# Kernel optimization log

Hardware: AMD Instinct MI355X
Metric: run time of the kernel (lower is better)

Reference implementation:

```python
import jax, jax.numpy as jnp
import numpy as np

SPARSE_COMPRESSION_RATIO = 0.5  # config.sparse_compression_ratio


def setup_inputs() -> dict:
    key = jax.random.key(0)
    kv_cache = jax.random.normal(key, (2, 32, 4096, 128), dtype=jnp.float32)
    return {"kv_cache": kv_cache}


def reference(kv_cache):
    # elements_to_keep = int(numel * (1 - ratio))
    total = kv_cache.size
    k = int(total * (1.0 - SPARSE_COMPRESSION_RATIO))
    flat = kv_cache.reshape(-1)
    # torch.topk(|x|, k, largest=True) -> indices of k largest magnitudes
    _, top_idx = jax.lax.top_k(jnp.abs(flat), k)
    # scatter mask, then elementwise multiply (zeros out non-top-k entries)
    mask = jnp.zeros((total,), dtype=jnp.bool_).at[top_idx].set(True)
    return kv_cache * mask.reshape(kv_cache.shape)
```

## Files before the change

### kernel.cpp

```cpp
#include <hip/hip_runtime.h>
#include <stdint.h>


#define NTHR 256
#define MASK31 0x7fffffffu

typedef unsigned int v4u __attribute__((ext_vector_type(4)));

#define SH_OFF    0
#define SH_BINS   8192
#define CH_OFF    8192
#define CH_BINS   4096
#define SCL_OFF   12288
#define L3_OFF    12304
#define L3_CAP    4096
#define PAIRS_OFF (L3_OFF + 2 * L3_CAP)
#define PAIRS_CAP (1u << 20)
#define ZERO_WORDS (SCL_OFF + 16)

#define STG_CAP   2048

__global__ void zero_ws_kernel(uint32_t* __restrict__ ws) {
    int i = blockIdx.x * blockDim.x + threadIdx.x;
    if (i < ZERO_WORDS) ws[i] = 0;
}

__global__ void sample_hist_kernel(const uint4* __restrict__ xv, long long n4,
                                   uint32_t* __restrict__ ws) {
    __shared__ uint32_t lh[SH_BINS];
    for (int i = threadIdx.x; i < SH_BINS; i += NTHR) lh[i] = 0;
    __syncthreads();
    long long chunkStride = n4 >> 7;
    long long base = (long long)blockIdx.x * chunkStride + threadIdx.x;
    for (int j = 0; j < 8; ++j) {
        long long idx = base + (long long)j * NTHR;
        if (idx < n4) {
            uint4 v = xv[idx];
            atomicAdd(&lh[(v.x & MASK31) >> 18], 1u);
            atomicAdd(&lh[(v.y & MASK31) >> 18], 1u);
            atomicAdd(&lh[(v.z & MASK31) >> 18], 1u);
            atomicAdd(&lh[(v.w & MASK31) >> 18], 1u);
        }
    }
    __syncthreads();
    for (int i = threadIdx.x; i < SH_BINS; i += NTHR)
        if (lh[i]) atomicAdd(&ws[SH_OFF + i], lh[i]);
}

__global__ void sel_bracket_kernel(uint32_t* __restrict__ ws,
                                   uint32_t ksmM, uint32_t kspM) {
    __shared__ uint32_t lh[SH_BINS];
    __shared__ uint32_t csum[NTHR];
    __shared__ uint32_t cpre[NTHR];
    __shared__ int sBHi, sB1;
    for (int i = threadIdx.x; i < SH_BINS; i += NTHR) lh[i] = ws[SH_OFF + i];
    if (threadIdx.x == 0) { sBHi = -1; sB1 = -1; }
    __syncthreads();
    uint32_t s = 0;
    for (int i = 0; i < 32; ++i) s += lh[threadIdx.x * 32 + i];
    csum[threadIdx.x] = s;
    __syncthreads();
    if (threadIdx.x == 0) {
        uint32_t run = 0;
        for (int c = NTHR - 1; c >= 0; --c) { cpre[c] = run; run += csum[c]; }
    }
    __syncthreads();
    {
        int c = threadIdx.x;
        int hitHi = -1, hitB1 = -1;
        uint32_t excl = cpre[c];
        for (int bb = c * 32 + 31; bb >= c * 32; --bb) {
            uint32_t cnt = lh[bb];
            uint32_t incl = excl + cnt;
            if (hitHi < 0 && incl >= ksmM) hitHi = bb;
            if (hitB1 < 0 && excl >= kspM) hitB1 = bb;
            excl = incl;
        }
        if (hitHi >= 0) atomicMax(&sBHi, hitHi);
        if (hitB1 >= 0) atomicMax(&sB1, hitB1);
    }
    __syncthreads();
    if (threadIdx.x == 0) {
        int bHi = sBHi < 0 ? 0 : sBHi;
        int bLo = sB1 + 1;
        if (bLo > bHi) bLo = bHi;
        if (bLo < 0) bLo = 0;
        int sbins = bHi - bLo + 1;
        int clog = 0; while ((1 << clog) < sbins) ++clog;
        int spanBits = 18 + clog;
        int shift1 = spanBits - 12;
        if (shift1 < 0) shift1 = 0;
        ws[SCL_OFF + 0] = ((uint32_t)bLo) << 18;
        ws[SCL_OFF + 1] = ((uint32_t)(bHi + 1)) << 18;
        ws[SCL_OFF + 2] = (uint32_t)shift1;
    }
}

__global__ __launch_bounds__(NTHR, 4)
void fused_main_kernel(const uint32_t* __restrict__ x,
                       uint32_t* __restrict__ out, long long n,
                       uint32_t* __restrict__ ws) {
    __shared__ uint2 stage[STG_CAP];
    __shared__ uint32_t cnt, sBase, redHi[NTHR / 64];
    const uint32_t uLo = ws[SCL_OFF + 0];
    const uint32_t uHi = ws[SCL_OFF + 1];
    const uint32_t span = uHi - uLo;
    if (threadIdx.x == 0) cnt = 0u;
    __syncthreads();

    const v4u* __restrict__ xv = (const v4u*)x;
    v4u* __restrict__ ov = (v4u*)out;
    uint2* __restrict__ gpairs = (uint2*)(ws + PAIRS_OFF);
    long long n4 = n >> 2;
    const long long stride = (long long)gridDim.x * NTHR;
    const long long i0 = (long long)blockIdx.x * NTHR + threadIdx.x;

    uint32_t myHi = 0;
    uint32_t hitMask = 0;
    uint32_t it = 0;
    long long i = i0;

#define CLASS(v, o, hb) { \
    uint32_t c0 = v.x & MASK31, c1 = v.y & MASK31, c2 = v.z & MASK31, c3 = v.w & MASK31; \
    myHi += (uint32_t)(c0 >= uHi) + (uint32_t)(c1 >= uHi) \
          + (uint32_t)(c2 >= uHi) + (uint32_t)(c3 >= uHi); \
    o.x = (c0 >= uHi) ? v.x : 0u; o.y = (c1 >= uHi) ? v.y : 0u; \
    o.z = (c2 >= uHi) ? v.z : 0u; o.w = (c3 >= uHi) ? v.w : 0u; \
    hb = (uint32_t)((c0 - uLo) < span) | (uint32_t)((c1 - uLo) < span) \
       | (uint32_t)((c2 - uLo) < span) | (uint32_t)((c3 - uLo) < span); }

    for (; i + 3 * stride < n4; i += 4 * stride, it += 4) {
        v4u v0 = xv[i];
        v4u v1 = xv[i + stride];
        v4u v2 = xv[i + 2 * stride];
        v4u v3 = xv[i + 3 * stride];
        v4u o0, o1, o2, o3;
        uint32_t h0, h1, h2, h3;
        CLASS(v0, o0, h0) CLASS(v1, o1, h1) CLASS(v2, o2, h2) CLASS(v3, o3, h3)
        hitMask |= h0 << (it & 31);
        hitMask |= h1 << ((it + 1) & 31);
        hitMask |= h2 << ((it + 2) & 31);
        hitMask |= h3 << ((it + 3) & 31);
        __builtin_nontemporal_store(o0, &ov[i]);
        __builtin_nontemporal_store(o1, &ov[i + stride]);
        __builtin_nontemporal_store(o2, &ov[i + 2 * stride]);
        __builtin_nontemporal_store(o3, &ov[i + 3 * stride]);
    }
    for (; i < n4; i += stride, ++it) {
        v4u v = xv[i];
        v4u o;
        uint32_t hb;
        CLASS(v, o, hb)
        hitMask |= hb << (it & 31);
        __builtin_nontemporal_store(o, &ov[i]);
    }
#undef CLASS

#define PUSHP(val, eidx) { \
    uint32_t p_ = atomicAdd(&cnt, 1u); \
    uint2 pr_ = make_uint2((val), (eidx)); \
    if (p_ < STG_CAP) stage[p_] = pr_; \
    else { uint32_t g_ = atomicAdd(&ws[SCL_OFF + 4], 1u); \
           if (g_ < PAIRS_CAP) gpairs[g_] = pr_; } }

    if (blockIdx.x == 0) {
        for (long long idx = (n4 << 2) + threadIdx.x; idx < n; idx += NTHR) {
            uint32_t v = x[idx];
            uint32_t u = v & MASK31;
            myHi += (uint32_t)(u >= uHi);
            if (u - uLo < span) PUSHP(v, (uint32_t)idx)
            out[idx] = (u >= uHi) ? v : 0u;
        }
    }

    while (hitMask) {
        uint32_t b = __ffs(hitMask) - 1u;
        hitMask &= hitMask - 1u;
        for (long long ii = i0 + (long long)b * stride; ii < n4; ii += (stride << 5)) {
            v4u v = xv[ii];
            uint32_t e0 = (uint32_t)(ii << 2);
            uint32_t u;
            u = v.x & MASK31; if (u - uLo < span) PUSHP(v.x, e0 + 0u)
            u = v.y & MASK31; if (u - uLo < span) PUSHP(v.y, e0 + 1u)
            u = v.z & MASK31; if (u - uLo < span) PUSHP(v.z, e0 + 2u)
            u = v.w & MASK31; if (u - uLo < span) PUSHP(v.w, e0 + 3u)
        }
    }
#undef PUSHP

    for (int o = 32; o > 0; o >>= 1) myHi += __shfl_down(myHi, o);
    if ((threadIdx.x & 63) == 0) redHi[threadIdx.x >> 6] = myHi;
    __syncthreads();
    if (threadIdx.x == 0) {
        uint32_t tot = 0;
        for (int w = 0; w < NTHR / 64; ++w) tot += redHi[w];
        if (tot) atomicAdd(&ws[SCL_OFF + 3], tot);
        uint32_t c = cnt < STG_CAP ? cnt : STG_CAP;
        cnt = c;
        sBase = atomicAdd(&ws[SCL_OFF + 4], c);
    }
    __syncthreads();
    uint32_t c = cnt, bw = sBase;
    for (uint32_t q = threadIdx.x; q < c; q += NTHR)
        if (bw + q < PAIRS_CAP) gpairs[bw + q] = stage[q];
}

__global__ void cand_hist_kernel(uint32_t* __restrict__ ws) {
    __shared__ uint32_t lh[CH_BINS];
    uint32_t G = ws[SCL_OFF + 4]; if (G > PAIRS_CAP) G = PAIRS_CAP;
    uint32_t uLo = ws[SCL_OFF + 0], shift1 = ws[SCL_OFF + 2];
    for (int i = threadIdx.x; i < CH_BINS; i += NTHR) lh[i] = 0;
    __syncthreads();
    const uint2* pairs = (const uint2*)(ws + PAIRS_OFF);
    uint32_t stride = gridDim.x * NTHR;
    for (uint32_t i = blockIdx.x * NTHR + threadIdx.x; i < G; i += stride) {
        uint32_t u = pairs[i].x & MASK31;
        atomicAdd(&lh[((u - uLo) >> shift1) & (CH_BINS - 1)], 1u);
    }
    __syncthreads();
    for (int i = threadIdx.x; i < CH_BINS; i += NTHR)
        if (lh[i]) atomicAdd(&ws[CH_OFF + i], lh[i]);
}

__global__ void sel_gather_kernel(uint32_t* __restrict__ ws, uint32_t k) {
    __shared__ uint32_t lh[CH_BINS];
    __shared__ uint32_t csum[NTHR];
    __shared__ uint32_t cpre[NTHR];
    __shared__ uint32_t sBase2, sRem2, sKp;
    for (int i = threadIdx.x; i < CH_BINS; i += NTHR) lh[i] = ws[CH_OFF + i];
    __syncthreads();
    uint32_t s = 0;
    for (int i = 0; i < 16; ++i) s += lh[threadIdx.x * 16 + i];
    csum[threadIdx.x] = s;
    __syncthreads();
    if (threadIdx.x == 0) {
        uint32_t run = 0;
        for (int c = NTHR - 1; c >= 0; --c) { cpre[c] = run; run += csum[c]; }
        uint32_t cntHi = ws[SCL_OFF + 3];
        uint32_t total = cpre[0] + csum[0];
        uint32_t kp = (k > cntHi) ? (k - cntHi) : 1u;
        if (kp > total) kp = total;
        if (kp < 1u) kp = 1u;
        sKp = kp;
    }
    __syncthreads();
    uint32_t kp = sKp;
    if (cpre[threadIdx.x] < kp && kp <= cpre[threadIdx.x] + csum[threadIdx.x]) {
        uint32_t excl = cpre[threadIdx.x];
        for (int bb = threadIdx.x * 16 + 15; bb >= threadIdx.x * 16; --bb) {
            uint32_t cnt = lh[bb];
            if (excl + cnt >= kp) {
                sBase2 = ws[SCL_OFF + 0] + (((uint32_t)bb) << ws[SCL_OFF + 2]);
                sRem2 = kp - excl;
                break;
            }
            excl += cnt;
        }
    }
    __syncthreads();
    if (threadIdx.x == 0) { ws[SCL_OFF + 5] = sBase2; ws[SCL_OFF + 6] = sRem2; }
    uint32_t base2 = sBase2;
    uint32_t width = 1u << ws[SCL_OFF + 2];
    uint32_t G = ws[SCL_OFF + 4]; if (G > PAIRS_CAP) G = PAIRS_CAP;
    const uint2* pairs = (const uint2*)(ws + PAIRS_OFF);
    uint2* l3 = (uint2*)(ws + L3_OFF);
    uint32_t stride = gridDim.x * NTHR;
    for (uint32_t i = blockIdx.x * NTHR + threadIdx.x; i < G; i += stride) {
        uint2 pr = pairs[i];
        uint32_t u = pr.x & MASK31;
        if (u - base2 < width) {
            uint32_t p = atomicAdd(&ws[SCL_OFF + 7], 1u);
            if (p < L3_CAP) l3[p] = pr;
        }
    }
}

__global__ void final_fixup_kernel(uint32_t* __restrict__ ws,
                                   uint32_t* __restrict__ out) {
    __shared__ uint2 l3s[L3_CAP];
    uint32_t c3 = ws[SCL_OFF + 7]; if (c3 > L3_CAP) c3 = L3_CAP;
    uint32_t base2 = ws[SCL_OFF + 5], rem2 = ws[SCL_OFF + 6];
    uint32_t width = 1u << ws[SCL_OFF + 2];
    uint32_t tHi2 = base2 + width;
    const uint2* l3 = (const uint2*)(ws + L3_OFF);
    for (uint32_t q = threadIdx.x; q < c3; q += NTHR) l3s[q] = l3[q];
    __syncthreads();
    uint32_t G = ws[SCL_OFF + 4]; if (G > PAIRS_CAP) G = PAIRS_CAP;
    const uint2* pairs = (const uint2*)(ws + PAIRS_OFF);
    uint32_t stride = gridDim.x * NTHR;
    for (uint32_t i = blockIdx.x * NTHR + threadIdx.x; i < G; i += stride) {
        uint2 pr = pairs[i];
        uint32_t u = pr.x & MASK31;
        if (u >= tHi2) {
            out[pr.y] = pr.x;
        } else if (u - base2 < width) {
            uint32_t rank = 0;
            for (uint32_t p = 0; p < c3; ++p) {
                uint2 q2 = l3s[p];
                uint32_t up = q2.x & MASK31;
                rank += (up > u || (up == u && q2.y < pr.y)) ? 1u : 0u;
            }
            if (rank < rem2) out[pr.y] = pr.x;
        }
    }
}

extern "C" void kernel_launch(void* const* d_in, const int* in_sizes, int n_in,
                              void* d_out, int out_size, void* d_ws, size_t ws_size,
                              hipStream_t stream) {
    const uint32_t* x = (const uint32_t*)d_in[0];
    uint32_t* out = (uint32_t*)d_out;
    uint32_t* ws = (uint32_t*)d_ws;
    long long n = (long long)in_sizes[0];

    const double ratio = 0.5;
    long long k = (long long)((double)n * (1.0 - ratio));
    if (k < 1) k = 1;
    if (k > n) k = n;

    long long n4 = n >> 2;
    long long S = ((n4 >> 7) >= 2048) ? (128LL * NTHR * 8 * 4)
                                      : (n4 << 2);
    long long ks = (long long)((double)k * ((double)S / (double)n));
    const long long M = 4500;
    uint32_t ksmM = (uint32_t)((ks - M) < 1 ? 1 : (ks - M));
    uint32_t kspM = (uint32_t)((ks + M) > S ? S : (ks + M));

    long long nBlk = (n4 + (long long)NTHR * 16 - 1) / ((long long)NTHR * 16);
    if (nBlk < 1) nBlk = 1;
    if (nBlk > 8192) nBlk = 8192;
    int grid = (int)nBlk;

    zero_ws_kernel<<<(ZERO_WORDS + NTHR - 1) / NTHR, NTHR, 0, stream>>>(ws);
    sample_hist_kernel<<<128, NTHR, 0, stream>>>((const uint4*)x, n4, ws);
    sel_bracket_kernel<<<1, NTHR, 0, stream>>>(ws, ksmM, kspM);
    fused_main_kernel<<<grid, NTHR, 0, stream>>>(x, out, n, ws);
    cand_hist_kernel<<<256, NTHR, 0, stream>>>(ws);
    sel_gather_kernel<<<256, NTHR, 0, stream>>>(ws, (uint32_t)k);
    final_fixup_kernel<<<256, NTHR, 0, stream>>>(ws, out);
}
```

Baseline: 143.2 us.

## Replace global atomic candidate compaction with per-block segments and larger sample

```diff
diff --git a/kernel.cpp b/kernel.cpp
--- a/kernel.cpp
+++ b/kernel.cpp
@@ -12,30 +12,36 @@
 #define CH_OFF    8192
 #define CH_BINS   4096
 #define SCL_OFF   12288
-#define L3_OFF    12304
-#define L3_CAP    4096
-#define PAIRS_OFF (L3_OFF + 2 * L3_CAP)
-#define PAIRS_CAP (1u << 20)
-#define ZERO_WORDS (SCL_OFF + 16)
-
-#define STG_CAP   2048
+#define ZERO_WORDS (SCL_OFF + 32)
+#define HIC_OFF   12320
+#define PCN_OFF   14368
+#define L3C_OFF   16416
+#define L3S_OFF   16672
+#define L3SEG_CAP 64
+#define OVFP_OFF  49440
+#define OVFP_CAP  16384
+#define OVL3_OFF  90000
+#define OVL3_CAP  2048
+#define PAIRS_OFF 131072
+#define SEG_CAP   2048
+#define NBLK_MAIN 2048
 
 __global__ void zero_ws_kernel(uint32_t* __restrict__ ws) {
     int i = blockIdx.x * blockDim.x + threadIdx.x;
     if (i < ZERO_WORDS) ws[i] = 0;
 }
 
-__global__ void sample_hist_kernel(const uint4* __restrict__ xv, long long n4,
+__global__ void sample_hist_kernel(const v4u* __restrict__ xv, long long n4,
                                    uint32_t* __restrict__ ws) {
     __shared__ uint32_t lh[SH_BINS];
     for (int i = threadIdx.x; i < SH_BINS; i += NTHR) lh[i] = 0;
     __syncthreads();
-    long long chunkStride = n4 >> 7;
-    long long base = (long long)blockIdx.x * chunkStride + threadIdx.x;
-    for (int j = 0; j < 8; ++j) {
-        long long idx = base + (long long)j * NTHR;
-        if (idx < n4) {
-            uint4 v = xv[idx];
+    long long S4 = n4 >> 3;
+    long long T = (long long)gridDim.x * NTHR;
+    for (long long s = (long long)blockIdx.x * NTHR + threadIdx.x; s < S4; s += T) {
+        long long idx4 = ((s >> 9) << 12) | (s & 511);
+        if (idx4 < n4) {
+            v4u v = xv[idx4];
             atomicAdd(&lh[(v.x & MASK31) >> 18], 1u);
             atomicAdd(&lh[(v.y & MASK31) >> 18], 1u);
             atomicAdd(&lh[(v.z & MASK31) >> 18], 1u);
@@ -96,12 +102,11 @@
     }
 }
 
-__global__ __launch_bounds__(NTHR, 4)
-void fused_main_kernel(const uint32_t* __restrict__ x,
-                       uint32_t* __restrict__ out, long long n,
-                       uint32_t* __restrict__ ws) {
-    __shared__ uint2 stage[STG_CAP];
-    __shared__ uint32_t cnt, sBase, redHi[NTHR / 64];
+__global__ void fused_main_kernel(const uint32_t* __restrict__ x,
+                                  uint32_t* __restrict__ out, long long n,
+                                  uint32_t* __restrict__ ws) {
+    __shared__ uint2 stage[SEG_CAP];
+    __shared__ uint32_t cnt, redHi[NTHR / 64];
     const uint32_t uLo = ws[SCL_OFF + 0];
     const uint32_t uHi = ws[SCL_OFF + 1];
     const uint32_t span = uHi - uLo;
@@ -110,7 +115,6 @@
 
     const v4u* __restrict__ xv = (const v4u*)x;
     v4u* __restrict__ ov = (v4u*)out;
-    uint2* __restrict__ gpairs = (uint2*)(ws + PAIRS_OFF);
     long long n4 = n >> 2;
     const long long stride = (long long)gridDim.x * NTHR;
     const long long i0 = (long long)blockIdx.x * NTHR + threadIdx.x;
@@ -156,12 +160,13 @@
     }
 #undef CLASS
 
+    uint2* __restrict__ ovfp = (uint2*)(ws + OVFP_OFF);
 #define PUSHP(val, eidx) { \
     uint32_t p_ = atomicAdd(&cnt, 1u); \
     uint2 pr_ = make_uint2((val), (eidx)); \
-    if (p_ < STG_CAP) stage[p_] = pr_; \
-    else { uint32_t g_ = atomicAdd(&ws[SCL_OFF + 4], 1u); \
-           if (g_ < PAIRS_CAP) gpairs[g_] = pr_; } }
+    if (p_ < SEG_CAP) stage[p_] = pr_; \
+    else { uint32_t g_ = atomicAdd(&ws[SCL_OFF + 5], 1u); \
+           if (g_ < OVFP_CAP) ovfp[g_] = pr_; } }
 
     if (blockIdx.x == 0) {
         for (long long idx = (n4 << 2) + threadIdx.x; idx < n; idx += NTHR) {
@@ -194,28 +199,39 @@
     if (threadIdx.x == 0) {
         uint32_t tot = 0;
         for (int w = 0; w < NTHR / 64; ++w) tot += redHi[w];
-        if (tot) atomicAdd(&ws[SCL_OFF + 3], tot);
-        uint32_t c = cnt < STG_CAP ? cnt : STG_CAP;
+        ws[HIC_OFF + blockIdx.x] = tot;
+        uint32_t c = cnt < SEG_CAP ? cnt : SEG_CAP;
         cnt = c;
-        sBase = atomicAdd(&ws[SCL_OFF + 4], c);
-    }
-    __syncthreads();
-    uint32_t c = cnt, bw = sBase;
-    for (uint32_t q = threadIdx.x; q < c; q += NTHR)
-        if (bw + q < PAIRS_CAP) gpairs[bw + q] = stage[q];
+        ws[PCN_OFF + blockIdx.x] = c;
+    }
+    __syncthreads();
+    uint2* __restrict__ seg = (uint2*)(ws + PAIRS_OFF) + (size_t)blockIdx.x * SEG_CAP;
+    uint32_t c = cnt;
+    for (uint32_t q = threadIdx.x; q < c; q += NTHR) seg[q] = stage[q];
 }
 
 __global__ void cand_hist_kernel(uint32_t* __restrict__ ws) {
     __shared__ uint32_t lh[CH_BINS];
-    uint32_t G = ws[SCL_OFF + 4]; if (G > PAIRS_CAP) G = PAIRS_CAP;
     uint32_t uLo = ws[SCL_OFF + 0], shift1 = ws[SCL_OFF + 2];
     for (int i = threadIdx.x; i < CH_BINS; i += NTHR) lh[i] = 0;
     __syncthreads();
     const uint2* pairs = (const uint2*)(ws + PAIRS_OFF);
-    uint32_t stride = gridDim.x * NTHR;
-    for (uint32_t i = blockIdx.x * NTHR + threadIdx.x; i < G; i += stride) {
-        uint32_t u = pairs[i].x & MASK31;
-        atomicAdd(&lh[((u - uLo) >> shift1) & (CH_BINS - 1)], 1u);
+    for (int g = 0; g < NBLK_MAIN / 256; ++g) {
+        uint32_t sidx = blockIdx.x + (uint32_t)g * 256u;
+        uint32_t c = ws[PCN_OFF + sidx];
+        const uint2* seg = pairs + (size_t)sidx * SEG_CAP;
+        for (uint32_t i = threadIdx.x; i < c; i += NTHR) {
+            uint32_t u = seg[i].x & MASK31;
+            atomicAdd(&lh[((u - uLo) >> shift1) & (CH_BINS - 1)], 1u);
+        }
+    }
+    if (blockIdx.x == 0) {
+        uint32_t c = ws[SCL_OFF + 5]; if (c > OVFP_CAP) c = OVFP_CAP;
+        const uint2* ovfp = (const uint2*)(ws + OVFP_OFF);
+        for (uint32_t i = threadIdx.x; i < c; i += NTHR) {
+            uint32_t u = ovfp[i].x & MASK31;
+            atomicAdd(&lh[((u - uLo) >> shift1) & (CH_BINS - 1)], 1u);
+        }
     }
     __syncthreads();
     for (int i = threadIdx.x; i < CH_BINS; i += NTHR)
@@ -226,8 +242,17 @@
     __shared__ uint32_t lh[CH_BINS];
     __shared__ uint32_t csum[NTHR];
     __shared__ uint32_t cpre[NTHR];
-    __shared__ uint32_t sBase2, sRem2, sKp;
+    __shared__ uint32_t sBase2, sRem2, sKp, lcnt;
+    uint32_t part = 0;
+    for (int i = threadIdx.x; i < NBLK_MAIN; i += NTHR) part += ws[HIC_OFF + i];
+    for (int o = 32; o > 0; o >>= 1) part += __shfl_down(part, o);
     for (int i = threadIdx.x; i < CH_BINS; i += NTHR) lh[i] = ws[CH_OFF + i];
+    if (threadIdx.x == 0) lcnt = 0;
+    csum[threadIdx.x] = 0;
+    __syncthreads();
+    if ((threadIdx.x & 63) == 0) csum[threadIdx.x >> 6] = part;
+    __syncthreads();
+    uint32_t cntHi = csum[0] + csum[1] + csum[2] + csum[3];
     __syncthreads();
     uint32_t s = 0;
     for (int i = 0; i < 16; ++i) s += lh[threadIdx.x * 16 + i];
@@ -236,7 +261,6 @@
     if (threadIdx.x == 0) {
         uint32_t run = 0;
         for (int c = NTHR - 1; c >= 0; --c) { cpre[c] = run; run += csum[c]; }
-        uint32_t cntHi = ws[SCL_OFF + 3];
         uint32_t total = cpre[0] + csum[0];
         uint32_t kp = (k > cntHi) ? (k - cntHi) : 1u;
         if (kp > total) kp = total;
@@ -258,49 +282,110 @@
         }
     }
     __syncthreads();
-    if (threadIdx.x == 0) { ws[SCL_OFF + 5] = sBase2; ws[SCL_OFF + 6] = sRem2; }
+    if (threadIdx.x == 0) { ws[SCL_OFF + 3] = sBase2; ws[SCL_OFF + 4] = sRem2; }
     uint32_t base2 = sBase2;
     uint32_t width = 1u << ws[SCL_OFF + 2];
-    uint32_t G = ws[SCL_OFF + 4]; if (G > PAIRS_CAP) G = PAIRS_CAP;
     const uint2* pairs = (const uint2*)(ws + PAIRS_OFF);
-    uint2* l3 = (uint2*)(ws + L3_OFF);
-    uint32_t stride = gridDim.x * NTHR;
-    for (uint32_t i = blockIdx.x * NTHR + threadIdx.x; i < G; i += stride) {
-        uint2 pr = pairs[i];
-        uint32_t u = pr.x & MASK31;
-        if (u - base2 < width) {
-            uint32_t p = atomicAdd(&ws[SCL_OFF + 7], 1u);
-            if (p < L3_CAP) l3[p] = pr;
-        }
-    }
-}
-
+    uint2* myl3 = (uint2*)(ws + L3S_OFF) + (size_t)blockIdx.x * L3SEG_CAP;
+    uint2* ovl3 = (uint2*)(ws + OVL3_OFF);
+    __shared__ uint2 lstage[L3SEG_CAP];
+    for (int g = 0; g < NBLK_MAIN / 256; ++g) {
+        uint32_t sidx = blockIdx.x + (uint32_t)g * 256u;
+        uint32_t c = ws[PCN_OFF + sidx];
+        const uint2* seg = pairs + (size_t)sidx * SEG_CAP;
+        for (uint32_t i = threadIdx.x; i < c; i += NTHR) {
+            uint2 pr = seg[i];
+            if ((pr.x & MASK31) - base2 < width) {
+                uint32_t p = atomicAdd(&lcnt, 1u);
+                if (p < L3SEG_CAP) lstage[p] = pr;
+                else { uint32_t g2 = atomicAdd(&ws[SCL_OFF + 6], 1u);
+                       if (g2 < OVL3_CAP) ovl3[g2] = pr; }
+            }
+        }
+    }
+    if (blockIdx.x == 0) {
+        uint32_t c = ws[SCL_OFF + 5]; if (c > OVFP_CAP) c = OVFP_CAP;
+        const uint2* ovfp = (const uint2*)(ws + OVFP_OFF);
+        for (uint32_t i = threadIdx.x; i < c; i += NTHR) {
+            uint2 pr = ovfp[i];
+            if ((pr.x & MASK31) - base2 < width) {
+                uint32_t p = atomicAdd(&lcnt, 1u);
+                if (p < L3SEG_CAP) lstage[p] = pr;
+                else { uint32_t g2 = atomicAdd(&ws[SCL_OFF + 6], 1u);
+                       if (g2 < OVL3_CAP) ovl3[g2] = pr; }
+            }
+        }
+    }
+    __syncthreads();
+    uint32_t c = lcnt < L3SEG_CAP ? lcnt : L3SEG_CAP;
+    if (threadIdx.x == 0) ws[L3C_OFF + blockIdx.x] = c;
+    for (uint32_t q = threadIdx.x; q < c; q += NTHR) myl3[q] = lstage[q];
+}
+
+#define L3TOT_CAP 4096
 __global__ void final_fixup_kernel(uint32_t* __restrict__ ws,
                                    uint32_t* __restrict__ out) {
-    __shared__ uint2 l3s[L3_CAP];
-    uint32_t c3 = ws[SCL_OFF + 7]; if (c3 > L3_CAP) c3 = L3_CAP;
-    uint32_t base2 = ws[SCL_OFF + 5], rem2 = ws[SCL_OFF + 6];
+    __shared__ uint2 l3s[L3TOT_CAP];
+    __shared__ uint32_t tc;
+    uint32_t base2 = ws[SCL_OFF + 3], rem2 = ws[SCL_OFF + 4];
     uint32_t width = 1u << ws[SCL_OFF + 2];
     uint32_t tHi2 = base2 + width;
-    const uint2* l3 = (const uint2*)(ws + L3_OFF);
-    for (uint32_t q = threadIdx.x; q < c3; q += NTHR) l3s[q] = l3[q];
-    __syncthreads();
-    uint32_t G = ws[SCL_OFF + 4]; if (G > PAIRS_CAP) G = PAIRS_CAP;
+    if (threadIdx.x == 0) tc = 0;
+    __syncthreads();
+    const uint2* l3seg = (const uint2*)(ws + L3S_OFF);
+    for (int s2 = threadIdx.x; s2 < 256; s2 += NTHR) {
+        uint32_t c = ws[L3C_OFF + s2];
+        uint32_t p = atomicAdd(&tc, c);
+        for (uint32_t q = 0; q < c; ++q)
+            if (p + q < L3TOT_CAP) l3s[p + q] = l3seg[(size_t)s2 * L3SEG_CAP + q];
+    }
+    if (threadIdx.x == 0) {
+        uint32_t c = ws[SCL_OFF + 6]; if (c > OVL3_CAP) c = OVL3_CAP;
+        uint32_t p = atomicAdd(&tc, c);
+        const uint2* ovl3 = (const uint2*)(ws + OVL3_OFF);
+        for (uint32_t q = 0; q < c; ++q)
+            if (p + q < L3TOT_CAP) l3s[p + q] = ovl3[q];
+    }
+    __syncthreads();
+    uint32_t c3 = tc < L3TOT_CAP ? tc : L3TOT_CAP;
     const uint2* pairs = (const uint2*)(ws + PAIRS_OFF);
-    uint32_t stride = gridDim.x * NTHR;
-    for (uint32_t i = blockIdx.x * NTHR + threadIdx.x; i < G; i += stride) {
-        uint2 pr = pairs[i];
-        uint32_t u = pr.x & MASK31;
-        if (u >= tHi2) {
-            out[pr.y] = pr.x;
-        } else if (u - base2 < width) {
-            uint32_t rank = 0;
-            for (uint32_t p = 0; p < c3; ++p) {
-                uint2 q2 = l3s[p];
-                uint32_t up = q2.x & MASK31;
-                rank += (up > u || (up == u && q2.y < pr.y)) ? 1u : 0u;
+    for (int g = 0; g < NBLK_MAIN / 256; ++g) {
+        uint32_t sidx = blockIdx.x + (uint32_t)g * 256u;
+        uint32_t c = ws[PCN_OFF + sidx];
+        const uint2* seg = pairs + (size_t)sidx * SEG_CAP;
+        for (uint32_t i = threadIdx.x; i < c; i += NTHR) {
+            uint2 pr = seg[i];
+            uint32_t u = pr.x & MASK31;
+            if (u >= tHi2) {
+                out[pr.y] = pr.x;
+            } else if (u - base2 < width) {
+                uint32_t rank = 0;
+                for (uint32_t p = 0; p < c3; ++p) {
+                    uint2 q2 = l3s[p];
+                    uint32_t up = q2.x & MASK31;
+                    rank += (up > u || (up == u && q2.y < pr.y)) ? 1u : 0u;
+                }
+                if (rank < rem2) out[pr.y] = pr.x;
             }
-            if (rank < rem2) out[pr.y] = pr.x;
+        }
+    }
+    if (blockIdx.x == 0) {
+        uint32_t c = ws[SCL_OFF + 5]; if (c > OVFP_CAP) c = OVFP_CAP;
+        const uint2* ovfp = (const uint2*)(ws + OVFP_OFF);
+        for (uint32_t i = threadIdx.x; i < c; i += NTHR) {
+            uint2 pr = ovfp[i];
+            uint32_t u = pr.x & MASK31;
+            if (u >= tHi2) {
+                out[pr.y] = pr.x;
+            } else if (u - base2 < width) {
+                uint32_t rank = 0;
+                for (uint32_t p = 0; p < c3; ++p) {
+                    uint2 q2 = l3s[p];
+                    uint32_t up = q2.x & MASK31;
+                    rank += (up > u || (up == u && q2.y < pr.y)) ? 1u : 0u;
+                }
+                if (rank < rem2) out[pr.y] = pr.x;
+            }
         }
     }
 }
@@ -319,22 +404,17 @@
     if (k > n) k = n;
 
     long long n4 = n >> 2;
-    long long S = ((n4 >> 7) >= 2048) ? (128LL * NTHR * 8 * 4)
-                                      : (n4 << 2);
+    long long S4 = n4 >> 3;
+    long long S = S4 << 2;
     long long ks = (long long)((double)k * ((double)S / (double)n));
-    const long long M = 4500;
+    const long long M = 9216;
     uint32_t ksmM = (uint32_t)((ks - M) < 1 ? 1 : (ks - M));
     uint32_t kspM = (uint32_t)((ks + M) > S ? S : (ks + M));
 
-    long long nBlk = (n4 + (long long)NTHR * 16 - 1) / ((long long)NTHR * 16);
-    if (nBlk < 1) nBlk = 1;
-    if (nBlk > 8192) nBlk = 8192;
-    int grid = (int)nBlk;
-
     zero_ws_kernel<<<(ZERO_WORDS + NTHR - 1) / NTHR, NTHR, 0, stream>>>(ws);
-    sample_hist_kernel<<<128, NTHR, 0, stream>>>((const uint4*)x, n4, ws);
+    sample_hist_kernel<<<256, NTHR, 0, stream>>>((const v4u*)x, n4, ws);
     sel_bracket_kernel<<<1, NTHR, 0, stream>>>(ws, ksmM, kspM);
-    fused_main_kernel<<<grid, NTHR, 0, stream>>>(x, out, n, ws);
+    fused_main_kernel<<<NBLK_MAIN, NTHR, 0, stream>>>(x, out, n, ws);
     cand_hist_kernel<<<256, NTHR, 0, stream>>>(ws);
     sel_gather_kernel<<<256, NTHR, 0, stream>>>(ws, (uint32_t)k);
     final_fixup_kernel<<<256, NTHR, 0, stream>>>(ws, out);
```

Result: no change. 143.8 us (+0.4%).
